# Performance work log

Hardware: AMD Instinct MI355X
Metric: run time of the kernel (lower is better)

## Reference

```python
import jax, jax.numpy as jnp
import numpy as np

B, T = 32, 25
TAU_M, TAU_S = 4.0, 1.0
TH, SG = 1.0, 4.0  # spike threshold, surrogate-gradient sharpness

@jax.custom_vjp
def spike_fn(v):
    return (v > TH).astype(v.dtype)

def _spike_fwd(v):
    return spike_fn(v), v

def _spike_bwd(v, g):
    s = jax.nn.sigmoid(SG * (v - TH))
    return (g * SG * s * (1.0 - s),)

spike_fn.defvjp(_spike_fwd, _spike_bwd)

def setup_inputs() -> dict:
    key = jax.random.key(0)
    ks = jax.random.split(key, 13)
    d = {}
    d["inputs"] = jax.random.normal(ks[0], (B, 3, 32, 32), jnp.float32)
    d["ann1_w"] = jax.random.normal(ks[1], (32, 3, 3, 3), jnp.float32) * 0.1
    d["ann1_b"] = jnp.zeros((32,), jnp.float32)
    d["w2"] = jax.random.normal(ks[2], (32, 32, 3, 3), jnp.float32) * 0.06
    d["b2"] = jnp.zeros((32,), jnp.float32)
    d["w3"] = jax.random.normal(ks[3], (64, 32, 3, 3), jnp.float32) * 0.06
    d["b3"] = jnp.zeros((64,), jnp.float32)
    d["w5"] = jax.random.normal(ks[4], (64, 64, 3, 3), jnp.float32) * 0.04
    d["b5"] = jnp.zeros((64,), jnp.float32)
    d["w7"] = jax.random.normal(ks[5], (512, 1600), jnp.float32) * (1.0 / np.sqrt(1600))
    d["b7"] = jnp.zeros((512,), jnp.float32)
    d["w8"] = jax.random.normal(ks[6], (10, 512), jnp.float32) * (1.0 / np.sqrt(512))
    d["b8"] = jnp.zeros((10,), jnp.float32)
    return d

def _conv(x, w, b):
    y = jax.lax.conv_general_dilated(x, w, (1, 1), 'VALID',
                                     dimension_numbers=('NCHW', 'OIHW', 'NCHW'))
    return y + b[None, :, None, None]

def _maxpool(x):
    return jax.lax.reduce_window(x, -jnp.inf, jax.lax.max,
                                 (1, 1, 2, 2), (1, 1, 2, 2), 'VALID')

def reference(inputs, ann1_w, ann1_b, w2, b2, w3, b3, w5, b5, w7, b7, w8, b8):
    eta_m = jnp.exp(jnp.asarray(-1.0 / TAU_M, jnp.float32))
    eta_s = jnp.exp(jnp.asarray(-1.0 / TAU_S, jnp.float32))
    a1, a2c = eta_m + eta_s, -eta_m * eta_s  # dual-exp IIR coefficients

    # ANN front-end, constant over time (expand_along_time just repeats it)
    frame = jax.nn.sigmoid(_conv(inputs, ann1_w, ann1_b))  # [B,32,30,30]

    def axon(x, st):  # second-order dual-exponential IIR synapse
        y1, y2 = st
        y = a1 * y1 + a2c * y2 + x
        return y, (y, y1)

    def lif(cur, st):  # LIF with membrane filter, zero-reset via prev spike
        v, s = st
        v_new = eta_m * v * (1.0 - s) + cur
        spk = spike_fn(v_new)
        return spk, (v_new, spk)

    def z(*shape):
        zz = jnp.zeros(shape, jnp.float32)
        return (zz, zz)

    carry0 = (z(B, 32, 30, 30), z(B, 32, 28, 28), z(B, 32, 28, 28),
              z(B, 64, 26, 26), z(B, 64, 26, 26), z(B, 64, 13, 13),
              z(B, 64, 11, 11), z(B, 64, 11, 11), z(B, 1600),
              z(B, 512), z(B, 512), z(B, 10))

    def step(carry, _):
        ax2, sn2, ax3, sn3, ax4, ax5, sn5, ax6, ax7, sn7, ax8, sn8 = carry
        a2o, ax2 = axon(frame, ax2)
        s2, sn2 = lif(_conv(a2o, w2, b2), sn2)
        a3o, ax3 = axon(s2, ax3)
        s3, sn3 = lif(_conv(a3o, w3, b3), sn3)
        a4o, ax4 = axon(s3, ax4)
        s4 = _maxpool(a4o)                       # [B,64,13,13]
        a5o, ax5 = axon(s4, ax5)
        s5, sn5 = lif(_conv(a5o, w5, b5), sn5)   # [B,64,11,11]
        a6o, ax6 = axon(s5, ax6)
        s6 = _maxpool(a6o)                       # [B,64,5,5]
        flat = s6.reshape(B, -1)                 # [B,1600]
        a7o, ax7 = axon(flat, ax7)
        s7, sn7 = lif(a7o @ w7.T + b7, sn7)      # [B,512]
        a8o, ax8 = axon(s7, ax8)
        s8, sn8 = lif(a8o @ w8.T + b8, sn8)      # [B,10]
        return (ax2, sn2, ax3, sn3, ax4, ax5, sn5, ax6, ax7, sn7, ax8, sn8), s8

    _, outs = jax.lax.scan(step, carry0, None, length=T)  # [T,B,10]
    return jnp.transpose(outs, (1, 2, 0))  # [B,10,T] matching torch time-last layout
```

## Files before the change

kernel.cpp:

```cpp
#include <hip/hip_runtime.h>
#include <math.h>


__device__ __forceinline__ float axon_step(float A1, float A2, float y1, float y2, float x) {
    return __fadd_rn(__fadd_rn(__fmul_rn(A1, y1), __fmul_rn(A2, y2)), x);
}

__global__ void diag_kernel(float* out, float v, int n) {
    int i = blockIdx.x * 256 + threadIdx.x;
    if (i < n) out[i] = v;
}

__global__ void canary_kernel(float* out, int n) {
    __shared__ float ssum[256];
    float s = 0.f;
    for (int i = threadIdx.x; i < n; i += 256) s += out[i];
    ssum[threadIdx.x] = s;
    __syncthreads();
    for (int k = 128; k > 0; k >>= 1) {
        if (threadIdx.x < k) ssum[threadIdx.x] += ssum[threadIdx.x + k];
        __syncthreads();
    }
    if (threadIdx.x == 0 && ssum[0] == 0.0f) out[0] = 444.0f;
}

__global__ __launch_bounds__(256) void wcvt_kernel(
        const float* __restrict__ w2, const float* __restrict__ w3,
        const float* __restrict__ w5,
        double* __restrict__ w2d, double* __restrict__ w3d,
        double* __restrict__ w5d) {
    int i = blockIdx.x * 256 + threadIdx.x;
    if (i < 9216)  w2d[i] = (double)w2[i];
    if (i < 18432) w3d[i] = (double)w3[i];
    if (i < 36864) w5d[i] = (double)w5[i];
}

__global__ __launch_bounds__(256) void ann1_kernel(
        const float* __restrict__ in, const float* __restrict__ w,
        const float* __restrict__ bias, float* __restrict__ frame) {
    int bid = blockIdx.x;
    int b = bid & 31, co = bid >> 5;
    int tid = threadIdx.x;
    __shared__ double wsh[27];
    if (tid < 27) wsh[tid] = (double)w[co * 27 + tid];
    __syncthreads();
    float bb = bias[co];
    for (int p = tid; p < 900; p += 256) {
        int y = p / 30, x = p % 30;
        double acc = 0.0;
        #pragma unroll
        for (int ci = 0; ci < 3; ++ci) {
            const float* r = in + ((b * 3 + ci) * 32 + y) * 32 + x;
            const double* wp = wsh + ci * 9;
            #pragma unroll
            for (int ky = 0; ky < 3; ++ky)
                acc += (double)r[ky*32+0]*wp[ky*3+0] + (double)r[ky*32+1]*wp[ky*3+1]
                     + (double)r[ky*32+2]*wp[ky*3+2];
        }
        float z = __fadd_rn((float)acc, bb);
        frame[((b * 32 + co) * 30 + y) * 30 + x] =
            (float)(1.0 / (1.0 + exp(-(double)z)));
    }
}

__global__ __launch_bounds__(256) void axon2g_kernel(
        const float2* __restrict__ frame2, float* __restrict__ a2ch,
        float A1, float A2) {
    int g = blockIdx.x * 256 + threadIdx.x;
    float2 f = frame2[g];
    float y1a = 0.f, y2a = 0.f, y1b = 0.f, y2b = 0.f;
    #pragma unroll
    for (int k = 0; k < 25; ++k) {
        float v0 = axon_step(A1, A2, y1a, y2a, f.x);
        float v1 = axon_step(A1, A2, y1b, y2b, f.y);
        ((float2*)(a2ch + (size_t)k * 921600))[g] = make_float2(v0, v1);
        y2a = y1a; y1a = v0;
        y2b = y1b; y1b = v1;
    }
}

template<bool FIRST>
__global__ __launch_bounds__(256) void axon2_kernel(
        const float2* __restrict__ frame2, float4* __restrict__ y2q,
        float2* __restrict__ a2o2, float A1, float A2) {
    int g = blockIdx.x * 256 + threadIdx.x;
    float2 f = frame2[g];
    float4 y = FIRST ? make_float4(0.f, 0.f, 0.f, 0.f) : y2q[g];
    float v0 = axon_step(A1, A2, y.x, y.y, f.x);
    float v1 = axon_step(A1, A2, y.z, y.w, f.y);
    y2q[g] = make_float4(v0, y.x, v1, y.z);
    a2o2[g] = make_float2(v0, v1);
}

template<bool FIRST>
__global__ __launch_bounds__(256) void conv2_kernel(
        const float* __restrict__ a2o, const double* __restrict__ w2d,
        const float* __restrict__ b2,
        float* __restrict__ w2st, float2* __restrict__ y3p,
        float* __restrict__ a3o, float A1, float A2, float eta_m) {
    int bid = blockIdx.x;
    int b = bid & 31, cop = (bid >> 5) & 15, sp = bid >> 9;
    int co0 = cop * 2;
    int row0 = sp * 14;
    int p = threadIdx.x;
    if (p >= 196) return;
    int lr = p / 14, xp = p % 14;
    int y = row0 + lr, x = xp * 2;
    double acc0[2] = {0.0, 0.0}, acc1[2] = {0.0, 0.0};
    const double* wbase = w2d + co0 * 288;
    #pragma unroll 2
    for (int ci = 0; ci < 32; ++ci) {
        const float* r = a2o + ((b * 32 + ci) * 30 + y) * 30 + x;
        const double* wp = wbase + ci * 9;
        #pragma unroll
        for (int ky = 0; ky < 3; ++ky) {
            float2 lo = *(const float2*)(r + ky * 30);
            float2 hi = *(const float2*)(r + ky * 30 + 2);
            double v0 = (double)lo.x, v1 = (double)lo.y;
            double v2 = (double)hi.x, v3 = (double)hi.y;
            #pragma unroll
            for (int j = 0; j < 2; ++j) {
                const double* wj = wp + j * 288 + ky * 3;
                acc0[j] += v0*wj[0] + v1*wj[1] + v2*wj[2];
                acc1[j] += v1*wj[0] + v2*wj[1] + v3*wj[2];
            }
        }
    }
    #pragma unroll
    for (int j = 0; j < 2; ++j) {
        int co = co0 + j;
        float bb = b2[co];
        #pragma unroll
        for (int u = 0; u < 2; ++u) {
            int idx = (b * 32 + co) * 784 + y * 28 + x + u;
            float cur = __fadd_rn((float)(u ? acc1[j] : acc0[j]), bb);
            float wprev = FIRST ? 0.f : w2st[idx];
            float vn = __fadd_rn(__fmul_rn(eta_m, wprev), cur);
            float sn = vn > 1.0f ? 1.0f : 0.0f;
            w2st[idx] = vn > 1.0f ? 0.0f : vn;
            float2 y3 = FIRST ? make_float2(0.f, 0.f) : y3p[idx];
            float yv = axon_step(A1, A2, y3.x, y3.y, sn);
            y3p[idx] = make_float2(yv, y3.x);
            a3o[idx] = yv;
        }
    }
}

template<bool FIRST>
__global__ __launch_bounds__(256) void conv3_kernel(
        const float* __restrict__ a3o, const double* __restrict__ w3d,
        const float* __restrict__ b3,
        float* __restrict__ w3st, float2* __restrict__ y4p,
        float2* __restrict__ y5p, float* __restrict__ a5o,
        float A1, float A2, float eta_m) {
    int bid = blockIdx.x;
    int b = bid & 31, coq = (bid >> 5) & 15, sp = bid >> 9;
    int co0 = coq * 4;
    int row0 = sp ? 14 : 0;
    int nrow = sp ? 12 : 14;
    int pr0  = sp ? 7 : 0;
    int npr  = sp ? 6 : 7;
    int tid = threadIdx.x;
    __shared__ float tile[4 * 364];
    int npair = nrow * 13;
    const double* wbase = w3d + co0 * 288;
    for (int p = tid; p < npair; p += 256) {
        int lr = p / 13, xp = p % 13;
        int y = row0 + lr, x = xp * 2;
        double acc0[4] = {0.0, 0.0, 0.0, 0.0};
        double acc1[4] = {0.0, 0.0, 0.0, 0.0};
        #pragma unroll 2
        for (int ci = 0; ci < 32; ++ci) {
            const float* r = a3o + ((b * 32 + ci) * 28 + y) * 28 + x;
            const double* wp = wbase + ci * 9;
            #pragma unroll
            for (int ky = 0; ky < 3; ++ky) {
                float2 lo = *(const float2*)(r + ky * 28);
                float2 hi = *(const float2*)(r + ky * 28 + 2);
                double v0 = (double)lo.x, v1 = (double)lo.y;
                double v2 = (double)hi.x, v3 = (double)hi.y;
                #pragma unroll
                for (int j = 0; j < 4; ++j) {
                    const double* wj = wp + j * 288 + ky * 3;
                    acc0[j] += v0*wj[0] + v1*wj[1] + v2*wj[2];
                    acc1[j] += v1*wj[0] + v2*wj[1] + v3*wj[2];
                }
            }
        }
        #pragma unroll
        for (int j = 0; j < 4; ++j) {
            int co = co0 + j;
            float bb = b3[co];
            #pragma unroll
            for (int u = 0; u < 2; ++u) {
                int idx = (b * 64 + co) * 676 + y * 26 + x + u;
                float cur = __fadd_rn((float)(u ? acc1[j] : acc0[j]), bb);
                float wprev = FIRST ? 0.f : w3st[idx];
                float vn = __fadd_rn(__fmul_rn(eta_m, wprev), cur);
                float sn = vn > 1.0f ? 1.0f : 0.0f;
                w3st[idx] = vn > 1.0f ? 0.0f : vn;
                float2 y4 = FIRST ? make_float2(0.f, 0.f) : y4p[idx];
                float a4 = axon_step(A1, A2, y4.x, y4.y, sn);
                y4p[idx] = make_float2(a4, y4.x);
                tile[j * 364 + lr * 26 + x + u] = a4;
            }
        }
    }
    __syncthreads();
    int npool = npr * 13 * 4;
    for (int q = tid; q < npool; q += 256) {
        int j = q / (npr * 13), pp = q % (npr * 13);
        int pry = pp / 13, px = pp % 13;
        int pr = pr0 + pry;
        int lr = 2 * pr - row0;
        const float* tp = tile + j * 364 + lr * 26 + 2 * px;
        float m = fmaxf(fmaxf(tp[0], tp[1]), fmaxf(tp[26], tp[27]));
        int idx = (b * 64 + co0 + j) * 169 + pr * 13 + px;
        float2 y5 = FIRST ? make_float2(0.f, 0.f) : y5p[idx];
        float yv = axon_step(A1, A2, y5.x, y5.y, m);
        y5p[idx] = make_float2(yv, y5.x);
        a5o[idx] = yv;
    }
}

template<bool FIRST>
__global__ __launch_bounds__(128) void conv5_kernel(
        const float* __restrict__ a5o, const double* __restrict__ w5d,
        const float* __restrict__ b5,
        float* __restrict__ w5st, float2* __restrict__ y6p,
        float2* __restrict__ y7p, float* __restrict__ a7o,
        float A1, float A2, float eta_m) {
    int bid = blockIdx.x;
    int b = bid & 31, co = bid >> 5;
    int tid = threadIdx.x;
    __shared__ float tile[121];
    const double* wbase = w5d + co * 576;
    if (tid < 121) {
        int y = tid / 11, x = tid % 11;
        double a[9] = {0,0,0,0,0,0,0,0,0};
        #pragma unroll 2
        for (int ci = 0; ci < 64; ++ci) {
            const float* r = a5o + (b * 64 + ci) * 169 + y * 13 + x;
            const double* wp = wbase + ci * 9;
            a[0] += (double)r[0]  * wp[0];
            a[1] += (double)r[1]  * wp[1];
            a[2] += (double)r[2]  * wp[2];
            a[3] += (double)r[13] * wp[3];
            a[4] += (double)r[14] * wp[4];
            a[5] += (double)r[15] * wp[5];
            a[6] += (double)r[26] * wp[6];
            a[7] += (double)r[27] * wp[7];
            a[8] += (double)r[28] * wp[8];
        }
        double acc = ((a[0]+a[1])+(a[2]+a[3])) + ((a[4]+a[5])+(a[6]+a[7])) + a[8];
        int idx = (b * 64 + co) * 121 + tid;
        float cur = __fadd_rn((float)acc, b5[co]);
        float wprev = FIRST ? 0.f : w5st[idx];
        float vn = __fadd_rn(__fmul_rn(eta_m, wprev), cur);
        float sn = vn > 1.0f ? 1.0f : 0.0f;
        w5st[idx] = vn > 1.0f ? 0.0f : vn;
        float2 y6 = FIRST ? make_float2(0.f, 0.f) : y6p[idx];
        float a6 = axon_step(A1, A2, y6.x, y6.y, sn);
        y6p[idx] = make_float2(a6, y6.x);
        tile[tid] = a6;
    }
    __syncthreads();
    if (tid < 25) {
        int py = tid / 5, px = tid % 5;
        const float* tp = tile + (2*py)*11 + 2*px;
        float m = fmaxf(fmaxf(tp[0], tp[1]), fmaxf(tp[11], tp[12]));
        int fi = b * 1600 + co * 25 + tid;
        float2 y7 = FIRST ? make_float2(0.f, 0.f) : y7p[fi];
        float yv = axon_step(A1, A2, y7.x, y7.y, m);
        y7p[fi] = make_float2(yv, y7.x);
        a7o[fi] = yv;
    }
}

template<bool FIRST>
__global__ __launch_bounds__(256) void fc7_kernel(
        const float* __restrict__ a7o, const float* __restrict__ w7,
        const float* __restrict__ b7,
        float* __restrict__ w7st, float2* __restrict__ y8p,
        float* __restrict__ a8o, float A1, float A2, float eta_m) {
    int bid = blockIdx.x;
    int b = bid & 31, ot = bid >> 5;
    int tid = threadIdx.x;
    int wave = tid >> 6, lane = tid & 63;
    __shared__ float sIn[1600];
    for (int i = tid; i < 1600; i += 256) sIn[i] = a7o[b * 1600 + i];
    __syncthreads();
    for (int oi = 0; oi < 4; ++oi) {
        int o = ot * 16 + wave * 4 + oi;
        const float* wr = w7 + o * 1600;
        double acc = 0.0;
        #pragma unroll
        for (int i = 0; i < 25; ++i)
            acc += (double)sIn[i * 64 + lane] * (double)wr[i * 64 + lane];
        #pragma unroll
        for (int off = 32; off > 0; off >>= 1)
            acc += __shfl_down(acc, off);
        if (lane == 0) {
            int idx = b * 512 + o;
            float cur = __fadd_rn((float)acc, b7[o]);
            float wprev = FIRST ? 0.f : w7st[idx];
            float vn = __fadd_rn(__fmul_rn(eta_m, wprev), cur);
            float sn = vn > 1.0f ? 1.0f : 0.0f;
            w7st[idx] = vn > 1.0f ? 0.0f : vn;
            float2 y8 = FIRST ? make_float2(0.f, 0.f) : y8p[idx];
            float yv = axon_step(A1, A2, y8.x, y8.y, sn);
            y8p[idx] = make_float2(yv, y8.x);
            a8o[idx] = yv;
        }
    }
}

template<bool FIRST>
__global__ __launch_bounds__(64) void fc8_kernel(
        const float* __restrict__ a8o, const float* __restrict__ w8,
        const float* __restrict__ b8, float* __restrict__ w8st,
        float* __restrict__ out, int t, float eta_m) {
    int b = blockIdx.x;
    int lane = threadIdx.x;
    const float* sr = a8o + b * 512;
    for (int o = 0; o < 10; ++o) {
        const float* wr = w8 + o * 512;
        double acc = 0.0;
        #pragma unroll
        for (int i = 0; i < 8; ++i)
            acc += (double)sr[i*64+lane] * (double)wr[i*64+lane];
        #pragma unroll
        for (int off = 32; off > 0; off >>= 1)
            acc += __shfl_down(acc, off);
        if (lane == 0) {
            int idx = b * 10 + o;
            float cur = __fadd_rn((float)acc, b8[o]);
            float wprev = FIRST ? 0.f : w8st[idx];
            float vn = __fadd_rn(__fmul_rn(eta_m, wprev), cur);
            float sn = vn > 1.0f ? 1.0f : 0.0f;
            w8st[idx] = vn > 1.0f ? 0.0f : vn;
            out[idx * 25 + t] = sn;
        }
    }
}

extern "C" void kernel_launch(void* const* d_in, const int* in_sizes, int n_in,
                              void* d_out, int out_size, void* d_ws, size_t ws_size,
                              hipStream_t stream) {
    (void)in_sizes; (void)n_in;
    const float* inp = (const float*)d_in[0];
    const float* a1w = (const float*)d_in[1];
    const float* a1b = (const float*)d_in[2];
    const float* w2  = (const float*)d_in[3];
    const float* b2  = (const float*)d_in[4];
    const float* w3  = (const float*)d_in[5];
    const float* b3  = (const float*)d_in[6];
    const float* w5  = (const float*)d_in[7];
    const float* b5  = (const float*)d_in[8];
    const float* w7  = (const float*)d_in[9];
    const float* b7  = (const float*)d_in[10];
    const float* w8  = (const float*)d_in[11];
    const float* b8  = (const float*)d_in[12];
    float* out = (float*)d_out;
    float* ws  = (float*)d_ws;

    const float em = (float)exp(-0.25);
    const float es = (float)exp(-1.0);
    const float A1 = em + es;
    const float A2 = -(em * es);

    size_t off = 0;
    auto nf = [&](size_t n) { size_t o = off; off += n; return o; };
    size_t o_w2d   = nf(2*9216);
    size_t o_w3d   = nf(2*18432);
    size_t o_w5d   = nf(2*36864);
    size_t o_frame = nf(921600);
    size_t o_a3o   = nf(802816);
    size_t o_a5o   = nf(346112);
    size_t o_a7o   = nf(51200);
    size_t o_a8o   = nf(16384);
    size_t o_w2st  = nf(802816);
    size_t o_y3p   = nf(2*802816);
    size_t o_w3st  = nf(1384448);
    size_t o_y4p   = nf(2*1384448);
    size_t o_y5p   = nf(2*346112);
    size_t o_w5st  = nf(247808);
    size_t o_y6p   = nf(2*247808);
    size_t o_y7p   = nf(2*51200);
    size_t o_w7st  = nf(16384);
    size_t o_y8p   = nf(2*16384);
    size_t o_w8st  = nf(320);
    size_t commonEnd = off;
    size_t o_a2ch  = commonEnd;
    size_t bigEnd  = commonEnd + (size_t)25 * 921600;
    size_t o_a2o   = commonEnd;
    size_t o_y2p   = commonEnd + 921600;
    size_t fbEnd   = commonEnd + 921600 + 2*921600;

    bool big = ws_size >= bigEnd * sizeof(float);
    if (!big && ws_size < fbEnd * sizeof(float)) {
        diag_kernel<<<(out_size + 255) / 256, 256, 0, stream>>>(
            out, 100.0f + (float)(ws_size >> 20), out_size);
        return;
    }

    wcvt_kernel<<<144, 256, 0, stream>>>(w2, w3, w5,
                                         (double*)(ws + o_w2d),
                                         (double*)(ws + o_w3d),
                                         (double*)(ws + o_w5d));
    ann1_kernel<<<1024, 256, 0, stream>>>(inp, a1w, a1b, ws + o_frame);

    if (big) {
        axon2g_kernel<<<1800, 256, 0, stream>>>((const float2*)(ws + o_frame),
                                                ws + o_a2ch, A1, A2);
    }

    for (int t = 0; t < 25; ++t) {
        const float* a2src;
        if (big) {
            a2src = ws + o_a2ch + (size_t)t * 921600;
        } else {
            if (t == 0)
                axon2_kernel<true><<<1800, 256, 0, stream>>>(
                    (const float2*)(ws + o_frame), (float4*)(ws + o_y2p),
                    (float2*)(ws + o_a2o), A1, A2);
            else
                axon2_kernel<false><<<1800, 256, 0, stream>>>(
                    (const float2*)(ws + o_frame), (float4*)(ws + o_y2p),
                    (float2*)(ws + o_a2o), A1, A2);
            a2src = ws + o_a2o;
        }
        if (t == 0) {
            conv2_kernel<true><<<1024, 256, 0, stream>>>(a2src, (const double*)(ws + o_w2d), b2,
                ws + o_w2st, (float2*)(ws + o_y3p), ws + o_a3o, A1, A2, em);
            conv3_kernel<true><<<1024, 256, 0, stream>>>(ws + o_a3o, (const double*)(ws + o_w3d), b3,
                ws + o_w3st, (float2*)(ws + o_y4p), (float2*)(ws + o_y5p), ws + o_a5o, A1, A2, em);
            conv5_kernel<true><<<2048, 128, 0, stream>>>(ws + o_a5o, (const double*)(ws + o_w5d), b5,
                ws + o_w5st, (float2*)(ws + o_y6p), (float2*)(ws + o_y7p), ws + o_a7o, A1, A2, em);
            fc7_kernel<true><<<1024, 256, 0, stream>>>(ws + o_a7o, w7, b7,
                ws + o_w7st, (float2*)(ws + o_y8p), ws + o_a8o, A1, A2, em);
            fc8_kernel<true><<<32, 64, 0, stream>>>(ws + o_a8o, w8, b8, ws + o_w8st,
                out, t, em);
        } else {
            conv2_kernel<false><<<1024, 256, 0, stream>>>(a2src, (const double*)(ws + o_w2d), b2,
                ws + o_w2st, (float2*)(ws + o_y3p), ws + o_a3o, A1, A2, em);
            conv3_kernel<false><<<1024, 256, 0, stream>>>(ws + o_a3o, (const double*)(ws + o_w3d), b3,
                ws + o_w3st, (float2*)(ws + o_y4p), (float2*)(ws + o_y5p), ws + o_a5o, A1, A2, em);
            conv5_kernel<false><<<2048, 128, 0, stream>>>(ws + o_a5o, (const double*)(ws + o_w5d), b5,
                ws + o_w5st, (float2*)(ws + o_y6p), (float2*)(ws + o_y7p), ws + o_a7o, A1, A2, em);
            fc7_kernel<false><<<1024, 256, 0, stream>>>(ws + o_a7o, w7, b7,
                ws + o_w7st, (float2*)(ws + o_y8p), ws + o_a8o, A1, A2, em);
            fc8_kernel<false><<<32, 64, 0, stream>>>(ws + o_a8o, w8, b8, ws + o_w8st,
                out, t, em);
        }
    }

    canary_kernel<<<1, 256, 0, stream>>>(out, out_size);
}
```

Before: 2.482 ms.

## Fold fc8 into next step's conv2 launch and split conv2/conv3 into smaller blocks

Removes the separate per-timestep fc8 launch by handling step t-1's fc8 in 32 extra blocks appended to step t's conv2 grid, with one final fc8 launch after the loop. conv2 and conv3 now use 128-thread blocks covering half as many rows, which doubles the grid to 2048 blocks and raises the ci unroll to 4. This is meant to cut launch overhead and improve occupancy and load balance. In exchange, rows overlap less between blocks, so more input is reloaded, and the conv3 tile split and the fused-block logic add complexity.

```diff
diff --git a/kernel.cpp b/kernel.cpp
--- a/kernel.cpp
+++ b/kernel.cpp
@@ -92,23 +92,53 @@
     a2o2[g] = make_float2(v0, v1);
 }
 
-template<bool FIRST>
-__global__ __launch_bounds__(256) void conv2_kernel(
+template<bool FIRST, bool FC8, bool FC8FIRST>
+__global__ __launch_bounds__(128) void conv2_kernel(
         const float* __restrict__ a2o, const double* __restrict__ w2d,
         const float* __restrict__ b2,
         float* __restrict__ w2st, float2* __restrict__ y3p,
-        float* __restrict__ a3o, float A1, float A2, float eta_m) {
+        float* __restrict__ a3o,
+        const float* __restrict__ a8o, const float* __restrict__ w8,
+        const float* __restrict__ b8, float* __restrict__ w8st,
+        float* __restrict__ outp, int tprev,
+        float A1, float A2, float eta_m) {
     int bid = blockIdx.x;
-    int b = bid & 31, cop = (bid >> 5) & 15, sp = bid >> 9;
+    if (FC8 && bid >= 2048) {
+        if (threadIdx.x >= 64) return;
+        int b = bid - 2048;
+        int lane = threadIdx.x;
+        const float* sr = a8o + b * 512;
+        for (int o = 0; o < 10; ++o) {
+            const float* wr = w8 + o * 512;
+            double acc = 0.0;
+            #pragma unroll
+            for (int i = 0; i < 8; ++i)
+                acc += (double)sr[i*64+lane] * (double)wr[i*64+lane];
+            #pragma unroll
+            for (int off = 32; off > 0; off >>= 1)
+                acc += __shfl_down(acc, off);
+            if (lane == 0) {
+                int idx = b * 10 + o;
+                float cur = __fadd_rn((float)acc, b8[o]);
+                float wprev = FC8FIRST ? 0.f : w8st[idx];
+                float vn = __fadd_rn(__fmul_rn(eta_m, wprev), cur);
+                float sn = vn > 1.0f ? 1.0f : 0.0f;
+                w8st[idx] = vn > 1.0f ? 0.0f : vn;
+                outp[idx * 25 + tprev] = sn;
+            }
+        }
+        return;
+    }
+    int b = bid & 31, cop = (bid >> 5) & 15, sp = (bid >> 9) & 3;
     int co0 = cop * 2;
-    int row0 = sp * 14;
+    int row0 = sp * 7;
     int p = threadIdx.x;
-    if (p >= 196) return;
+    if (p >= 98) return;
     int lr = p / 14, xp = p % 14;
     int y = row0 + lr, x = xp * 2;
     double acc0[2] = {0.0, 0.0}, acc1[2] = {0.0, 0.0};
     const double* wbase = w2d + co0 * 288;
-    #pragma unroll 2
+    #pragma unroll 4
     for (int ci = 0; ci < 32; ++ci) {
         const float* r = a2o + ((b * 32 + ci) * 30 + y) * 30 + x;
         const double* wp = wbase + ci * 9;
@@ -147,29 +177,29 @@
 }
 
 template<bool FIRST>
-__global__ __launch_bounds__(256) void conv3_kernel(
+__global__ __launch_bounds__(128) void conv3_kernel(
         const float* __restrict__ a3o, const double* __restrict__ w3d,
         const float* __restrict__ b3,
         float* __restrict__ w3st, float2* __restrict__ y4p,
         float2* __restrict__ y5p, float* __restrict__ a5o,
         float A1, float A2, float eta_m) {
     int bid = blockIdx.x;
-    int b = bid & 31, coq = (bid >> 5) & 15, sp = bid >> 9;
+    int b = bid & 31, coq = (bid >> 5) & 15, sp = (bid >> 9) & 3;
     int co0 = coq * 4;
-    int row0 = sp ? 14 : 0;
-    int nrow = sp ? 12 : 14;
-    int pr0  = sp ? 7 : 0;
-    int npr  = sp ? 6 : 7;
+    int pr0 = (sp == 0) ? 0 : (4 + 3 * (sp - 1));
+    int npr = (sp == 0) ? 4 : 3;
+    int row0 = 2 * pr0;
+    int nrow = 2 * npr;
     int tid = threadIdx.x;
-    __shared__ float tile[4 * 364];
+    __shared__ float tile[4 * 208];
     int npair = nrow * 13;
     const double* wbase = w3d + co0 * 288;
-    for (int p = tid; p < npair; p += 256) {
-        int lr = p / 13, xp = p % 13;
+    if (tid < npair) {
+        int lr = tid / 13, xp = tid % 13;
         int y = row0 + lr, x = xp * 2;
         double acc0[4] = {0.0, 0.0, 0.0, 0.0};
         double acc1[4] = {0.0, 0.0, 0.0, 0.0};
-        #pragma unroll 2
+        #pragma unroll 4
         for (int ci = 0; ci < 32; ++ci) {
             const float* r = a3o + ((b * 32 + ci) * 28 + y) * 28 + x;
             const double* wp = wbase + ci * 9;
@@ -202,18 +232,17 @@
                 float2 y4 = FIRST ? make_float2(0.f, 0.f) : y4p[idx];
                 float a4 = axon_step(A1, A2, y4.x, y4.y, sn);
                 y4p[idx] = make_float2(a4, y4.x);
-                tile[j * 364 + lr * 26 + x + u] = a4;
+                tile[j * 208 + lr * 26 + x + u] = a4;
             }
         }
     }
     __syncthreads();
     int npool = npr * 13 * 4;
-    for (int q = tid; q < npool; q += 256) {
+    for (int q = tid; q < npool; q += 128) {
         int j = q / (npr * 13), pp = q % (npr * 13);
         int pry = pp / 13, px = pp % 13;
         int pr = pr0 + pry;
-        int lr = 2 * pr - row0;
-        const float* tp = tile + j * 364 + lr * 26 + 2 * px;
+        const float* tp = tile + j * 208 + (2 * pry) * 26 + 2 * px;
         float m = fmaxf(fmaxf(tp[0], tp[1]), fmaxf(tp[26], tp[27]));
         int idx = (b * 64 + co0 + j) * 169 + pr * 13 + px;
         float2 y5 = FIRST ? make_float2(0.f, 0.f) : y5p[idx];
@@ -415,6 +444,10 @@
                                                 ws + o_a2ch, A1, A2);
     }
 
+    const double* w2dp = (const double*)(ws + o_w2d);
+    const double* w3dp = (const double*)(ws + o_w3d);
+    const double* w5dp = (const double*)(ws + o_w5d);
+
     for (int t = 0; t < 25; ++t) {
         const float* a2src;
         if (big) {
@@ -431,29 +464,36 @@
             a2src = ws + o_a2o;
         }
         if (t == 0) {
-            conv2_kernel<true><<<1024, 256, 0, stream>>>(a2src, (const double*)(ws + o_w2d), b2,
-                ws + o_w2st, (float2*)(ws + o_y3p), ws + o_a3o, A1, A2, em);
-            conv3_kernel<true><<<1024, 256, 0, stream>>>(ws + o_a3o, (const double*)(ws + o_w3d), b3,
+            conv2_kernel<true, false, false><<<2048, 128, 0, stream>>>(
+                a2src, w2dp, b2, ws + o_w2st, (float2*)(ws + o_y3p), ws + o_a3o,
+                ws + o_a8o, w8, b8, ws + o_w8st, out, -1, A1, A2, em);
+        } else if (t == 1) {
+            conv2_kernel<false, true, true><<<2080, 128, 0, stream>>>(
+                a2src, w2dp, b2, ws + o_w2st, (float2*)(ws + o_y3p), ws + o_a3o,
+                ws + o_a8o, w8, b8, ws + o_w8st, out, t - 1, A1, A2, em);
+        } else {
+            conv2_kernel<false, true, false><<<2080, 128, 0, stream>>>(
+                a2src, w2dp, b2, ws + o_w2st, (float2*)(ws + o_y3p), ws + o_a3o,
+                ws + o_a8o, w8, b8, ws + o_w8st, out, t - 1, A1, A2, em);
+        }
+        if (t == 0) {
+            conv3_kernel<true><<<2048, 128, 0, stream>>>(ws + o_a3o, w3dp, b3,
                 ws + o_w3st, (float2*)(ws + o_y4p), (float2*)(ws + o_y5p), ws + o_a5o, A1, A2, em);
-            conv5_kernel<true><<<2048, 128, 0, stream>>>(ws + o_a5o, (const double*)(ws + o_w5d), b5,
+            conv5_kernel<true><<<2048, 128, 0, stream>>>(ws + o_a5o, w5dp, b5,
                 ws + o_w5st, (float2*)(ws + o_y6p), (float2*)(ws + o_y7p), ws + o_a7o, A1, A2, em);
             fc7_kernel<true><<<1024, 256, 0, stream>>>(ws + o_a7o, w7, b7,
                 ws + o_w7st, (float2*)(ws + o_y8p), ws + o_a8o, A1, A2, em);
-            fc8_kernel<true><<<32, 64, 0, stream>>>(ws + o_a8o, w8, b8, ws + o_w8st,
-                out, t, em);
         } else {
-            conv2_kernel<false><<<1024, 256, 0, stream>>>(a2src, (const double*)(ws + o_w2d), b2,
-                ws + o_w2st, (float2*)(ws + o_y3p), ws + o_a3o, A1, A2, em);
-            conv3_kernel<false><<<1024, 256, 0, stream>>>(ws + o_a3o, (const double*)(ws + o_w3d), b3,
+            conv3_kernel<false><<<2048, 128, 0, stream>>>(ws + o_a3o, w3dp, b3,
                 ws + o_w3st, (float2*)(ws + o_y4p), (float2*)(ws + o_y5p), ws + o_a5o, A1, A2, em);
-            conv5_kernel<false><<<2048, 128, 0, stream>>>(ws + o_a5o, (const double*)(ws + o_w5d), b5,
+            conv5_kernel<false><<<2048, 128, 0, stream>>>(ws + o_a5o, w5dp, b5,
                 ws + o_w5st, (float2*)(ws + o_y6p), (float2*)(ws + o_y7p), ws + o_a7o, A1, A2, em);
             fc7_kernel<false><<<1024, 256, 0, stream>>>(ws + o_a7o, w7, b7,
                 ws + o_w7st, (float2*)(ws + o_y8p), ws + o_a8o, A1, A2, em);
-            fc8_kernel<false><<<32, 64, 0, stream>>>(ws + o_a8o, w8, b8, ws + o_w8st,
-                out, t, em);
-        }
-    }
+        }
+    }
+    fc8_kernel<false><<<32, 64, 0, stream>>>(ws + o_a8o, w8, b8, ws + o_w8st,
+                                             out, 24, em);
 
     canary_kernel<<<1, 256, 0, stream>>>(out, out_size);
 }
```

After: 2.611 ms. +5.2%, slower.
